# Kernel optimization log

Measured on AMD Instinct MI355X. Metric: run time of the kernel, lower is better.

## Reference

```python
import jax, jax.numpy as jnp
import numpy as np

DIM_Q = 512
DIM_K = 512
DIM_V = 512
NUM_HEADS = 8
LN_EPS = 1e-5


def setup_inputs() -> dict:
    key = jax.random.key(0)
    ks = jax.random.split(key, 12)
    s_q = 1.0 / np.sqrt(DIM_Q)
    s_k = 1.0 / np.sqrt(DIM_K)
    s_v = 1.0 / np.sqrt(DIM_V)
    return {
        "Q": jax.random.normal(ks[0], (8, 1024, DIM_Q), dtype=jnp.float32),
        "K": jax.random.normal(ks[1], (8, 1024, DIM_K), dtype=jnp.float32),
        "Wq": jax.random.uniform(ks[2], (DIM_Q, DIM_V), jnp.float32, -s_q, s_q),
        "bq": jax.random.uniform(ks[3], (DIM_V,), jnp.float32, -s_q, s_q),
        "Wk": jax.random.uniform(ks[4], (DIM_K, DIM_V), jnp.float32, -s_k, s_k),
        "bk": jax.random.uniform(ks[5], (DIM_V,), jnp.float32, -s_k, s_k),
        "Wv": jax.random.uniform(ks[6], (DIM_K, DIM_V), jnp.float32, -s_k, s_k),
        "bv": jax.random.uniform(ks[7], (DIM_V,), jnp.float32, -s_k, s_k),
        "Wo": jax.random.uniform(ks[8], (DIM_V, DIM_V), jnp.float32, -s_v, s_v),
        "bo": jax.random.uniform(ks[9], (DIM_V,), jnp.float32, -s_v, s_v),
        "g0": jnp.ones((DIM_V,), jnp.float32),
        "b0": jnp.zeros((DIM_V,), jnp.float32),
        "g1": jnp.ones((DIM_V,), jnp.float32),
        "b1": jnp.zeros((DIM_V,), jnp.float32),
    }


def _layer_norm(x, gamma, beta):
    mu = jnp.mean(x, axis=-1, keepdims=True)
    var = jnp.var(x, axis=-1, keepdims=True)
    return (x - mu) * jax.lax.rsqrt(var + LN_EPS) * gamma + beta


def reference(Q, K, Wq, bq, Wk, bk, Wv, bv, Wo, bo, g0, b0, g1, b1):
    B, Nq, _ = Q.shape
    Nk = K.shape[1]
    H = NUM_HEADS
    d = DIM_V // H  # head dim

    Qp = Q @ Wq + bq                      # [B, Nq, dim_V]
    Kp = K @ Wk + bk                      # [B, Nk, dim_V]
    Vp = K @ Wv + bv                      # [B, Nk, dim_V]

    Qh = Qp.reshape(B, Nq, H, d)
    Kh = Kp.reshape(B, Nk, H, d)
    Vh = Vp.reshape(B, Nk, H, d)

    scores = jnp.einsum("bqhd,bkhd->bhqk", Qh, Kh) / jnp.sqrt(jnp.float32(d))
    A = jax.nn.softmax(scores, axis=-1)   # [B, H, Nq, Nk]
    Oh = jnp.einsum("bhqk,bkhd->bqhd", A, Vh) + Qh  # residual with projected Q
    O = Oh.reshape(B, Nq, DIM_V)

    O = _layer_norm(O, g0, b0)
    O = O + jax.nn.relu(O @ Wo + bo)
    O = _layer_norm(O, g1, b1)
    return O
```

## Files before the change

### kernel.cpp

```cpp
#include <hip/hip_runtime.h>
#include <math.h>

#define DV 512
#define HD 64
#define NHEADS 8
#define SEQ 1024
#define NBATCH 8
#define MROWS (NBATCH * SEQ)

typedef __bf16 bf16;
typedef __bf16 bf16x8 __attribute__((ext_vector_type(8)));
typedef __bf16 bf16x4 __attribute__((ext_vector_type(4)));
typedef float f32x4 __attribute__((ext_vector_type(4)));

__device__ inline void gload_lds16(const void* g, void* l) {
  __builtin_amdgcn_global_load_lds(
      (const __attribute__((address_space(1))) unsigned int*)g,
      (__attribute__((address_space(3))) unsigned int*)l, 16, 0, 0);
}

__device__ __forceinline__ bf16x8 cvt8(float4 a, float4 b) {
  bf16x8 o;
  o[0] = (bf16)a.x; o[1] = (bf16)a.y; o[2] = (bf16)a.z; o[3] = (bf16)a.w;
  o[4] = (bf16)b.x; o[5] = (bf16)b.y; o[6] = (bf16)b.z; o[7] = (bf16)b.w;
  return o;
}

__global__ __launch_bounds__(256) void prep_w(
    const float* __restrict__ W0, const float* __restrict__ W1,
    const float* __restrict__ W2, const float* __restrict__ W3,
    bf16* __restrict__ T0, bf16* __restrict__ T1,
    bf16* __restrict__ T2, bf16* __restrict__ T3)
{
  const int z = blockIdx.z;
  const float* W = z == 0 ? W0 : z == 1 ? W1 : z == 2 ? W2 : W3;
  bf16* WT = z == 0 ? T0 : z == 1 ? T1 : z == 2 ? T2 : T3;
  __shared__ float T[64][65];
  const int t = threadIdx.x;
  const int k0 = (blockIdx.x >> 3) * 64, n0 = (blockIdx.x & 7) * 64;
#pragma unroll
  for (int p = 0; p < 4; ++p) {
    int r = p * 16 + (t >> 4), c = (t & 15) * 4;
    float4 v = *(const float4*)&W[(size_t)(k0 + r) * DV + n0 + c];
    T[r][c] = v.x; T[r][c + 1] = v.y; T[r][c + 2] = v.z; T[r][c + 3] = v.w;
  }
  __syncthreads();
#pragma unroll
  for (int p = 0; p < 2; ++p) {
    int n = p * 32 + (t >> 3), kc = (t & 7) * 8;
    bf16x8 o;
#pragma unroll
    for (int j = 0; j < 8; ++j) o[j] = (bf16)T[kc + j][n];
    *(bf16x8*)&WT[(size_t)(n0 + n) * DV + k0 + kc] = o;
  }
}

template<bool SA>
__device__ __forceinline__ void proj_core(
    const float* __restrict__ Sg, const bf16* __restrict__ Wg,
    int s0, int w0, float* Sf, bf16* Wb, f32x4 (*acc)[4])
{
  const int tid = threadIdx.x;
  const int lane = tid & 63, w = tid >> 6;
  const int wm = w >> 1, wn = w & 1;
  const int cl = lane & 15, qd = lane >> 4;
  const int sw = SA ? wm : wn;
  const int ww = SA ? wn : wm;

  size_t offS[4]; int uS[4];
#pragma unroll
  for (int t = 0; t < 4; ++t) {
    int S = t * 256 + tid;
    int row = S >> 3, g = (S & 7) ^ (row & 7);
    offS[t] = (size_t)(s0 + row) * DV + g * 4;
    uS[t] = (t * 256 + w * 64) * 4;
  }
  size_t offW[2]; int uW[2];
#pragma unroll
  for (int t = 0; t < 2; ++t) {
    int S = t * 256 + tid;
    int row = S >> 2, g = (S & 3) ^ ((row >> 1) & 3);
    offW[t] = (size_t)(w0 + row) * DV + g * 8;
    uW[t] = (t * 256 + w * 64) * 8;
  }

#pragma unroll
  for (int t = 0; t < 4; ++t) gload_lds16(Sg + offS[t], Sf + uS[t]);
#pragma unroll
  for (int t = 0; t < 2; ++t) gload_lds16(Wg + offW[t], Wb + uW[t]);

  for (int it = 0; it < 16; ++it) {
    __syncthreads();
    const int cur = it & 1;
    if (it + 1 < 16) {
      const size_t kn = (size_t)(it + 1) * 32;
#pragma unroll
      for (int t = 0; t < 4; ++t)
        gload_lds16(Sg + kn + offS[t], Sf + (cur ^ 1) * 4096 + uS[t]);
#pragma unroll
      for (int t = 0; t < 2; ++t)
        gload_lds16(Wg + kn + offW[t], Wb + (cur ^ 1) * 4096 + uW[t]);
    }
    const float* S_ = Sf + cur * 4096;
    const bf16* W_ = Wb + cur * 4096;

    bf16x8 sf[4], wf[4];
#pragma unroll
    for (int j = 0; j < 4; ++j) {
      int row = sw * 64 + j * 16 + cl;
      int lo = row * 8 + ((2 * qd) ^ (row & 7));
      int hi = row * 8 + ((2 * qd + 1) ^ (row & 7));
      float4 a = *(const float4*)(S_ + lo * 4);
      float4 b = *(const float4*)(S_ + hi * 4);
      sf[j] = cvt8(a, b);
    }
#pragma unroll
    for (int j = 0; j < 4; ++j) {
      int row = ww * 64 + j * 16 + cl;
      int slot = row * 4 + (qd ^ ((row >> 1) & 3));
      wf[j] = *(const bf16x8*)(W_ + (size_t)slot * 8);
    }
#pragma unroll
    for (int mi = 0; mi < 4; ++mi)
#pragma unroll
      for (int ni = 0; ni < 4; ++ni) {
        if (SA)
          acc[mi][ni] = __builtin_amdgcn_mfma_f32_16x16x32_bf16(
              sf[mi], wf[ni], acc[mi][ni], 0, 0, 0);
        else
          acc[mi][ni] = __builtin_amdgcn_mfma_f32_16x16x32_bf16(
              wf[mi], sf[ni], acc[mi][ni], 0, 0, 0);
      }
  }
}

__global__ __launch_bounds__(256) void gemm_proj(
    const float* __restrict__ Qf, const float* __restrict__ Kf,
    const bf16* __restrict__ WqT, const bf16* __restrict__ WkT,
    const bf16* __restrict__ WvT,
    const float* __restrict__ bq, const float* __restrict__ bk,
    const float* __restrict__ bv,
    bf16* __restrict__ Qp, bf16* __restrict__ Kp, bf16* __restrict__ VpT)
{
  __shared__ float Sf[2 * 4096];
  __shared__ bf16 Wb[2 * 4096];
  const int z = blockIdx.z;
  int m0, n0, N;
  f32x4 acc[4][4] = {};
  if (z < 2) {
    m0 = (blockIdx.x & 63) * 128; n0 = (blockIdx.x >> 6) * 128; N = DV;
    proj_core<true>(z ? Kf : Qf, z ? WkT : WqT, m0, n0, Sf, Wb, acc);
  } else {
    n0 = (blockIdx.x & 63) * 128; m0 = (blockIdx.x >> 6) * 128; N = MROWS;
    proj_core<false>(Kf, WvT, n0, m0, Sf, Wb, acc);
  }

  const float* bias = z == 0 ? bq : z == 1 ? bk : bv;
  bf16* C = z == 0 ? Qp : z == 1 ? Kp : VpT;
  const int lane = threadIdx.x & 63, w = threadIdx.x >> 6;
  const int wm = w >> 1, wn = w & 1;
  const int cl = lane & 15, qd = lane >> 4;
  float bcol[4] = {0.f, 0.f, 0.f, 0.f};
  if (z < 2)
#pragma unroll
    for (int ni = 0; ni < 4; ++ni) bcol[ni] = bias[n0 + wn * 64 + ni * 16 + cl];
#pragma unroll
  for (int mi = 0; mi < 4; ++mi)
#pragma unroll
    for (int r = 0; r < 4; ++r) {
      int gm = m0 + wm * 64 + mi * 16 + qd * 4 + r;
      float brow = (z == 2) ? bias[gm] : 0.f;
#pragma unroll
      for (int ni = 0; ni < 4; ++ni) {
        int gn = n0 + wn * 64 + ni * 16 + cl;
        float v = acc[mi][ni][r] + (z == 2 ? brow : bcol[ni]);
        C[(size_t)gm * N + gn] = (bf16)v;
      }
    }
}

__global__ __launch_bounds__(256) void attn_mfma(
    const bf16* __restrict__ Qp, const bf16* __restrict__ Kp,
    const bf16* __restrict__ VpT, bf16* __restrict__ Orb)
{
  __shared__ bf16 Ks[2][64 * 64];
  __shared__ bf16 Vs[2][64 * 64];
  __shared__ bf16 Ps[4][32 * 72];

  const int tid = threadIdx.x, lane = tid & 63, w = tid >> 6;
  const int cl = lane & 15, qd = lane >> 4;
  const int bh = blockIdx.x, b = bh >> 3, h = bh & 7;
  const int q0w = blockIdx.y * 128 + w * 32;

  const float SCL = 0.18033688011112042f;
  bf16x8 qa[2][2];
#pragma unroll
  for (int qt = 0; qt < 2; ++qt)
#pragma unroll
    for (int ch = 0; ch < 2; ++ch) {
      bf16x8 v = *(const bf16x8*)(Qp + ((size_t)b * SEQ + q0w + qt * 16 + cl) * DV
                                  + h * HD + ch * 32 + qd * 8);
#pragma unroll
      for (int j = 0; j < 8; ++j) v[j] = (bf16)((float)v[j] * SCL);
      qa[qt][ch] = v;
    }

  f32x4 o[4][2] = {};
  float lrun[2] = {0.f, 0.f};

  const bf16* Kbase = Kp + (size_t)b * SEQ * DV + h * HD;
  const bf16* Vbase = VpT + (size_t)h * HD * MROWS + (size_t)b * SEQ;
  bf16* Pw = &Ps[w][0];

  const int Sa = tid, Sb = 256 + tid;
  const int kRowA = Sa >> 3, kDgA = (Sa & 7) ^ (kRowA & 7);
  const int kRowB = Sb >> 3, kDgB = (Sb & 7) ^ (kRowB & 7);
  const size_t kOffA = (size_t)kRowA * DV + kDgA * 8;
  const size_t kOffB = (size_t)kRowB * DV + kDgB * 8;
  const size_t vOffA = (size_t)kRowA * MROWS + kDgA * 8;
  const size_t vOffB = (size_t)kRowB * MROWS + kDgB * 8;

  gload_lds16(Kbase + kOffA, &Ks[0][(size_t)(w * 64) * 8]);
  gload_lds16(Kbase + kOffB, &Ks[0][(size_t)(256 + w * 64) * 8]);
  gload_lds16(Vbase + vOffA, &Vs[0][(size_t)(w * 64) * 8]);
  gload_lds16(Vbase + vOffB, &Vs[0][(size_t)(256 + w * 64) * 8]);

  for (int it = 0; it < SEQ / 64; ++it) {
    __syncthreads();
    const int cur = it & 1;
    if (it + 1 < SEQ / 64) {
      const size_t kt = (size_t)(it + 1) * 64;
      gload_lds16(Kbase + kt * DV + kOffA, &Ks[cur ^ 1][(size_t)(w * 64) * 8]);
      gload_lds16(Kbase + kt * DV + kOffB, &Ks[cur ^ 1][(size_t)(256 + w * 64) * 8]);
      gload_lds16(Vbase + kt + vOffA, &Vs[cur ^ 1][(size_t)(w * 64) * 8]);
      gload_lds16(Vbase + kt + vOffB, &Vs[cur ^ 1][(size_t)(256 + w * 64) * 8]);
    }
    const bf16* K_ = &Ks[cur][0];
    const bf16* V_ = &Vs[cur][0];

    f32x4 sc[4][2] = {};
#pragma unroll
    for (int ch = 0; ch < 2; ++ch) {
      bf16x8 kf[4];
#pragma unroll
      for (int kt4 = 0; kt4 < 4; ++kt4) {
        int key = kt4 * 16 + cl;
        int slot = key * 8 + ((ch * 4 + qd) ^ (key & 7));
        kf[kt4] = *(const bf16x8*)(K_ + (size_t)slot * 8);
      }
#pragma unroll
      for (int kt4 = 0; kt4 < 4; ++kt4)
#pragma unroll
        for (int qt = 0; qt < 2; ++qt)
          sc[kt4][qt] = __builtin_amdgcn_mfma_f32_16x16x32_bf16(
              kf[kt4], qa[qt][ch], sc[kt4][qt], 0, 0, 0);
    }

#pragma unroll
    for (int qt = 0; qt < 2; ++qt) {
      float sum = 0.f;
#pragma unroll
      for (int kt4 = 0; kt4 < 4; ++kt4) {
        float p0 = __builtin_amdgcn_exp2f(sc[kt4][qt][0]);
        float p1 = __builtin_amdgcn_exp2f(sc[kt4][qt][1]);
        float p2 = __builtin_amdgcn_exp2f(sc[kt4][qt][2]);
        float p3 = __builtin_amdgcn_exp2f(sc[kt4][qt][3]);
        sum += (p0 + p1) + (p2 + p3);
        bf16x4 pk;
        pk[0] = (bf16)p0; pk[1] = (bf16)p1; pk[2] = (bf16)p2; pk[3] = (bf16)p3;
        *(bf16x4*)(Pw + (size_t)(qt * 16 + cl) * 72 + kt4 * 16 + qd * 4) = pk;
      }
      sum += __shfl_xor(sum, 16);
      sum += __shfl_xor(sum, 32);
      lrun[qt] += sum;
    }

#pragma unroll
    for (int kc = 0; kc < 2; ++kc) {
      bf16x8 pb[2];
#pragma unroll
      for (int qt = 0; qt < 2; ++qt)
        pb[qt] = *(const bf16x8*)(Pw + (size_t)(qt * 16 + cl) * 72 + kc * 32 + qd * 8);
#pragma unroll
      for (int dt = 0; dt < 4; ++dt) {
        int d = dt * 16 + cl;
        int slot = d * 8 + ((kc * 4 + qd) ^ (d & 7));
        bf16x8 vf = *(const bf16x8*)(V_ + (size_t)slot * 8);
#pragma unroll
        for (int qt = 0; qt < 2; ++qt)
          o[dt][qt] = __builtin_amdgcn_mfma_f32_16x16x32_bf16(
              vf, pb[qt], o[dt][qt], 0, 0, 0);
      }
    }
  }

#pragma unroll
  for (int qt = 0; qt < 2; ++qt) {
    float inv = 1.f / lrun[qt];
    size_t rowoff = ((size_t)b * SEQ + q0w + qt * 16 + cl) * DV + h * HD;
#pragma unroll
    for (int dt = 0; dt < 4; ++dt) {
      bf16x4 rv = *(const bf16x4*)(Qp + rowoff + dt * 16 + qd * 4);
      bf16x4 st;
      st[0] = (bf16)(o[dt][qt][0] * inv + (float)rv[0]);
      st[1] = (bf16)(o[dt][qt][1] * inv + (float)rv[1]);
      st[2] = (bf16)(o[dt][qt][2] * inv + (float)rv[2]);
      st[3] = (bf16)(o[dt][qt][3] * inv + (float)rv[3]);
      *(bf16x4*)(Orb + rowoff + dt * 16 + qd * 4) = st;
    }
  }
}

__global__ __launch_bounds__(256) void gemm_fused(
    const bf16* __restrict__ Orb, const bf16* __restrict__ WoT,
    const float* __restrict__ bo,
    const float* __restrict__ g0, const float* __restrict__ b0,
    const float* __restrict__ g1, const float* __restrict__ b1,
    float* __restrict__ out)
{
  __shared__ bf16 Bsm[32 * 512];
  __shared__ bf16 As[2][2048 * 8];
  const int tid = threadIdx.x, lane = tid & 63, w = tid >> 6;
  const int cl = lane & 15, qd = lane >> 4;
  const int m0 = blockIdx.x * 32;

  size_t offA[8];
  int uOff[8];
#pragma unroll
  for (int t = 0; t < 8; ++t) {
    int S = t * 256 + tid;
    int frow = S >> 2, kq = (S & 3) ^ ((frow >> 1) & 3);
    offA[t] = (size_t)frow * DV + kq * 8;
    uOff[t] = (t * 256 + w * 64) * 8;
  }

#pragma unroll
  for (int t = 0; t < 8; ++t)
    gload_lds16(WoT + offA[t], As[0] + uOff[t]);

  {
    const int q = tid >> 3, c0 = (tid & 7) * 64;
    const bf16* src = Orb + (size_t)(m0 + q) * DV + c0;
    float x[64];
    float s = 0.f, s2 = 0.f;
#pragma unroll
    for (int j = 0; j < 8; ++j) {
      bf16x8 xv = *(const bf16x8*)(src + j * 8);
#pragma unroll
      for (int e = 0; e < 8; ++e) {
        float f = (float)xv[e];
        x[j * 8 + e] = f; s += f; s2 += f * f;
      }
    }
    s  += __shfl_xor(s, 1);  s  += __shfl_xor(s, 2);  s  += __shfl_xor(s, 4);
    s2 += __shfl_xor(s2, 1); s2 += __shfl_xor(s2, 2); s2 += __shfl_xor(s2, 4);
    float mu = s * (1.f / DV);
    float inv = rsqrtf(s2 * (1.f / DV) - mu * mu + 1e-5f);
#pragma unroll
    for (int j = 0; j < 8; ++j) {
      float4 ga = *(const float4*)(g0 + c0 + j * 8);
      float4 gb = *(const float4*)(g0 + c0 + j * 8 + 4);
      float4 ba = *(const float4*)(b0 + c0 + j * 8);
      float4 bb = *(const float4*)(b0 + c0 + j * 8 + 4);
      bf16x8 o;
      o[0] = (bf16)((x[j*8+0] - mu) * inv * ga.x + ba.x);
      o[1] = (bf16)((x[j*8+1] - mu) * inv * ga.y + ba.y);
      o[2] = (bf16)((x[j*8+2] - mu) * inv * ga.z + ba.z);
      o[3] = (bf16)((x[j*8+3] - mu) * inv * ga.w + ba.w);
      o[4] = (bf16)((x[j*8+4] - mu) * inv * gb.x + bb.x);
      o[5] = (bf16)((x[j*8+5] - mu) * inv * gb.y + bb.y);
      o[6] = (bf16)((x[j*8+6] - mu) * inv * gb.z + bb.z);
      o[7] = (bf16)((x[j*8+7] - mu) * inv * gb.w + bb.w);
      int g = (tid & 7) * 8 + j;
      int slot = q * 64 + (g ^ (q & 7));
      *(bf16x8*)(Bsm + (size_t)slot * 8) = o;
    }
  }

  f32x4 acc[8][2] = {};
  for (int it = 0; it < 16; ++it) {
    __syncthreads();
    const int cur = it & 1;
    if (it + 1 < 16) {
#pragma unroll
      for (int t = 0; t < 8; ++t)
        gload_lds16(WoT + (size_t)(it + 1) * 32 + offA[t], As[cur ^ 1] + uOff[t]);
    }
    bf16x8 bfr[2];
#pragma unroll
    for (int nt = 0; nt < 2; ++nt) {
      int q = nt * 16 + cl;
      int slot = q * 64 + ((it * 4 + qd) ^ (q & 7));
      bfr[nt] = *(const bf16x8*)(Bsm + (size_t)slot * 8);
    }
#pragma unroll
    for (int mt = 0; mt < 8; ++mt) {
      int frow = (w * 8 + mt) * 16 + cl;
      int slot = frow * 4 + (qd ^ ((frow >> 1) & 3));
      bf16x8 af = *(const bf16x8*)(As[cur] + (size_t)slot * 8);
#pragma unroll
      for (int nt = 0; nt < 2; ++nt)
        acc[mt][nt] = __builtin_amdgcn_mfma_f32_16x16x32_bf16(
            af, bfr[nt], acc[mt][nt], 0, 0, 0);
    }
  }

  __syncthreads();
  float* red = (float*)As;
  float y[8][2][4];
  float sy[2], sy2[2];
#pragma unroll
  for (int nt = 0; nt < 2; ++nt) {
    sy[nt] = 0.f; sy2[nt] = 0.f;
    const int q = nt * 16 + cl;
#pragma unroll
    for (int mt = 0; mt < 8; ++mt) {
      const int f0 = (w * 8 + mt) * 16 + qd * 4;
      float4 bov = *(const float4*)(bo + f0);
      int g = f0 >> 3;
      int slot = q * 64 + (g ^ (q & 7));
      bf16x4 rv = *(const bf16x4*)(Bsm + (size_t)slot * 8 + (qd & 1) * 4);
      const float* bp = (const float*)&bov;
#pragma unroll
      for (int r = 0; r < 4; ++r) {
        float v = fmaxf(acc[mt][nt][r] + bp[r], 0.f) + (float)rv[r];
        y[mt][nt][r] = v;
        sy[nt] += v; sy2[nt] += v * v;
      }
    }
    sy[nt]  += __shfl_xor(sy[nt], 16);  sy[nt]  += __shfl_xor(sy[nt], 32);
    sy2[nt] += __shfl_xor(sy2[nt], 16); sy2[nt] += __shfl_xor(sy2[nt], 32);
  }
  if (qd == 0) {
#pragma unroll
    for (int nt = 0; nt < 2; ++nt) {
      int q = nt * 16 + cl;
      red[(q * 4 + w) * 2 + 0] = sy[nt];
      red[(q * 4 + w) * 2 + 1] = sy2[nt];
    }
  }
  __syncthreads();
#pragma unroll
  for (int nt = 0; nt < 2; ++nt) {
    const int q = nt * 16 + cl;
    float s = 0.f, s2 = 0.f;
#pragma unroll
    for (int ww = 0; ww < 4; ++ww) {
      s  += red[(q * 4 + ww) * 2 + 0];
      s2 += red[(q * 4 + ww) * 2 + 1];
    }
    float mu1 = s * (1.f / DV);
    float inv1 = rsqrtf(s2 * (1.f / DV) - mu1 * mu1 + 1e-5f);
    size_t rowoff = (size_t)(m0 + q) * DV;
#pragma unroll
    for (int mt = 0; mt < 8; ++mt) {
      const int f0 = (w * 8 + mt) * 16 + qd * 4;
      float4 gv = *(const float4*)(g1 + f0);
      float4 bv = *(const float4*)(b1 + f0);
      float4 ov;
      ov.x = (y[mt][nt][0] - mu1) * inv1 * gv.x + bv.x;
      ov.y = (y[mt][nt][1] - mu1) * inv1 * gv.y + bv.y;
      ov.z = (y[mt][nt][2] - mu1) * inv1 * gv.z + bv.z;
      ov.w = (y[mt][nt][3] - mu1) * inv1 * gv.w + bv.w;
      *(float4*)(out + rowoff + f0) = ov;
    }
  }
}

extern "C" void kernel_launch(void* const* d_in, const int* in_sizes, int n_in,
                              void* d_out, int out_size, void* d_ws, size_t ws_size,
                              hipStream_t stream)
{
  const float* Q  = (const float*)d_in[0];
  const float* Kf = (const float*)d_in[1];
  const float* Wq = (const float*)d_in[2];
  const float* bq = (const float*)d_in[3];
  const float* Wk = (const float*)d_in[4];
  const float* bk = (const float*)d_in[5];
  const float* Wv = (const float*)d_in[6];
  const float* bv = (const float*)d_in[7];
  const float* Wo = (const float*)d_in[8];
  const float* bo = (const float*)d_in[9];
  const float* g0 = (const float*)d_in[10];
  const float* b0 = (const float*)d_in[11];
  const float* g1 = (const float*)d_in[12];
  const float* b1 = (const float*)d_in[13];
  float* out = (float*)d_out;

  const size_t MB = 1ull << 20;
  char* W = (char*)d_ws;
  bf16* Orb = (bf16*)(W + 0);
  bf16* Qp  = (bf16*)(W + 8 * MB);
  bf16* Kp  = (bf16*)(W + 16 * MB);
  bf16* VpT = (bf16*)(W + 24 * MB);
  bf16* WqT = (bf16*)(W + 32 * MB);
  bf16* WkT = (bf16*)(W + 32 * MB + 512 * 1024);
  bf16* WvT = (bf16*)(W + 33 * MB);
  bf16* WoT = (bf16*)(W + 33 * MB + 512 * 1024);

  dim3 blk(256);
  prep_w<<<dim3(64, 1, 4), blk, 0, stream>>>(Wq, Wk, Wv, Wo, WqT, WkT, WvT, WoT);
  gemm_proj<<<dim3(256, 1, 3), blk, 0, stream>>>(
      Q, Kf, WqT, WkT, WvT, bq, bk, bv, Qp, Kp, VpT);
  attn_mfma<<<dim3(NBATCH * NHEADS, SEQ / 128), blk, 0, stream>>>(Qp, Kp, VpT, Orb);
  gemm_fused<<<dim3(MROWS / 32), blk, 0, stream>>>(
      Orb, WoT, bo, g0, b0, g1, b1, out);
}
```

Before: 188.8 us.

## Fuse K and V projections into one block sharing the K input tile

The K and V projections are merged into the same thread block, so each K tile is loaded from global memory and converted to bf16 once and then feeds both the Wk and Wv products. The grid drops from three z-slices to two, and z=1 blocks do twice the MFMA work with a second accumulator set and a second LDS weight buffer. This removes redundant reads and conversions of K, but it doubles accumulator registers (which may hurt occupancy) and leaves an imbalance between z=0 and z=1 blocks.

```diff
diff --git a/kernel.cpp b/kernel.cpp
--- a/kernel.cpp
+++ b/kernel.cpp
@@ -55,85 +55,6 @@
   }
 }
 
-template<bool SA>
-__device__ __forceinline__ void proj_core(
-    const float* __restrict__ Sg, const bf16* __restrict__ Wg,
-    int s0, int w0, float* Sf, bf16* Wb, f32x4 (*acc)[4])
-{
-  const int tid = threadIdx.x;
-  const int lane = tid & 63, w = tid >> 6;
-  const int wm = w >> 1, wn = w & 1;
-  const int cl = lane & 15, qd = lane >> 4;
-  const int sw = SA ? wm : wn;
-  const int ww = SA ? wn : wm;
-
-  size_t offS[4]; int uS[4];
-#pragma unroll
-  for (int t = 0; t < 4; ++t) {
-    int S = t * 256 + tid;
-    int row = S >> 3, g = (S & 7) ^ (row & 7);
-    offS[t] = (size_t)(s0 + row) * DV + g * 4;
-    uS[t] = (t * 256 + w * 64) * 4;
-  }
-  size_t offW[2]; int uW[2];
-#pragma unroll
-  for (int t = 0; t < 2; ++t) {
-    int S = t * 256 + tid;
-    int row = S >> 2, g = (S & 3) ^ ((row >> 1) & 3);
-    offW[t] = (size_t)(w0 + row) * DV + g * 8;
-    uW[t] = (t * 256 + w * 64) * 8;
-  }
-
-#pragma unroll
-  for (int t = 0; t < 4; ++t) gload_lds16(Sg + offS[t], Sf + uS[t]);
-#pragma unroll
-  for (int t = 0; t < 2; ++t) gload_lds16(Wg + offW[t], Wb + uW[t]);
-
-  for (int it = 0; it < 16; ++it) {
-    __syncthreads();
-    const int cur = it & 1;
-    if (it + 1 < 16) {
-      const size_t kn = (size_t)(it + 1) * 32;
-#pragma unroll
-      for (int t = 0; t < 4; ++t)
-        gload_lds16(Sg + kn + offS[t], Sf + (cur ^ 1) * 4096 + uS[t]);
-#pragma unroll
-      for (int t = 0; t < 2; ++t)
-        gload_lds16(Wg + kn + offW[t], Wb + (cur ^ 1) * 4096 + uW[t]);
-    }
-    const float* S_ = Sf + cur * 4096;
-    const bf16* W_ = Wb + cur * 4096;
-
-    bf16x8 sf[4], wf[4];
-#pragma unroll
-    for (int j = 0; j < 4; ++j) {
-      int row = sw * 64 + j * 16 + cl;
-      int lo = row * 8 + ((2 * qd) ^ (row & 7));
-      int hi = row * 8 + ((2 * qd + 1) ^ (row & 7));
-      float4 a = *(const float4*)(S_ + lo * 4);
-      float4 b = *(const float4*)(S_ + hi * 4);
-      sf[j] = cvt8(a, b);
-    }
-#pragma unroll
-    for (int j = 0; j < 4; ++j) {
-      int row = ww * 64 + j * 16 + cl;
-      int slot = row * 4 + (qd ^ ((row >> 1) & 3));
-      wf[j] = *(const bf16x8*)(W_ + (size_t)slot * 8);
-    }
-#pragma unroll
-    for (int mi = 0; mi < 4; ++mi)
-#pragma unroll
-      for (int ni = 0; ni < 4; ++ni) {
-        if (SA)
-          acc[mi][ni] = __builtin_amdgcn_mfma_f32_16x16x32_bf16(
-              sf[mi], wf[ni], acc[mi][ni], 0, 0, 0);
-        else
-          acc[mi][ni] = __builtin_amdgcn_mfma_f32_16x16x32_bf16(
-              wf[mi], sf[ni], acc[mi][ni], 0, 0, 0);
-      }
-  }
-}
-
 __global__ __launch_bounds__(256) void gemm_proj(
     const float* __restrict__ Qf, const float* __restrict__ Kf,
     const bf16* __restrict__ WqT, const bf16* __restrict__ WkT,
@@ -143,40 +64,138 @@
     bf16* __restrict__ Qp, bf16* __restrict__ Kp, bf16* __restrict__ VpT)
 {
   __shared__ float Sf[2 * 4096];
-  __shared__ bf16 Wb[2 * 4096];
+  __shared__ bf16 W1[2 * 4096];
+  __shared__ bf16 W2[2 * 4096];
   const int z = blockIdx.z;
-  int m0, n0, N;
-  f32x4 acc[4][4] = {};
-  if (z < 2) {
-    m0 = (blockIdx.x & 63) * 128; n0 = (blockIdx.x >> 6) * 128; N = DV;
-    proj_core<true>(z ? Kf : Qf, z ? WkT : WqT, m0, n0, Sf, Wb, acc);
-  } else {
-    n0 = (blockIdx.x & 63) * 128; m0 = (blockIdx.x >> 6) * 128; N = MROWS;
-    proj_core<false>(Kf, WvT, n0, m0, Sf, Wb, acc);
-  }
-
-  const float* bias = z == 0 ? bq : z == 1 ? bk : bv;
-  bf16* C = z == 0 ? Qp : z == 1 ? Kp : VpT;
-  const int lane = threadIdx.x & 63, w = threadIdx.x >> 6;
+  const int tid = threadIdx.x;
+  const int lane = tid & 63, w = tid >> 6;
   const int wm = w >> 1, wn = w & 1;
   const int cl = lane & 15, qd = lane >> 4;
-  float bcol[4] = {0.f, 0.f, 0.f, 0.f};
-  if (z < 2)
-#pragma unroll
-    for (int ni = 0; ni < 4; ++ni) bcol[ni] = bias[n0 + wn * 64 + ni * 16 + cl];
-#pragma unroll
-  for (int mi = 0; mi < 4; ++mi)
-#pragma unroll
-    for (int r = 0; r < 4; ++r) {
-      int gm = m0 + wm * 64 + mi * 16 + qd * 4 + r;
-      float brow = (z == 2) ? bias[gm] : 0.f;
-#pragma unroll
-      for (int ni = 0; ni < 4; ++ni) {
-        int gn = n0 + wn * 64 + ni * 16 + cl;
-        float v = acc[mi][ni][r] + (z == 2 ? brow : bcol[ni]);
-        C[(size_t)gm * N + gn] = (bf16)v;
-      }
-    }
+  const int s0 = (blockIdx.x & 63) * 128;
+  const int w0 = (blockIdx.x >> 6) * 128;
+
+  const float* Sg = z ? Kf : Qf;
+  const bf16* Wg1 = z ? WkT : WqT;
+
+  size_t offS[4]; int uS[4];
+#pragma unroll
+  for (int t = 0; t < 4; ++t) {
+    int S = t * 256 + tid;
+    int row = S >> 3, g = (S & 7) ^ (row & 7);
+    offS[t] = (size_t)(s0 + row) * DV + g * 4;
+    uS[t] = (t * 256 + w * 64) * 4;
+  }
+  size_t offW[2]; int uW[2];
+#pragma unroll
+  for (int t = 0; t < 2; ++t) {
+    int S = t * 256 + tid;
+    int row = S >> 2, g = (S & 3) ^ ((row >> 1) & 3);
+    offW[t] = (size_t)(w0 + row) * DV + g * 8;
+    uW[t] = (t * 256 + w * 64) * 8;
+  }
+
+#pragma unroll
+  for (int t = 0; t < 4; ++t) gload_lds16(Sg + offS[t], Sf + uS[t]);
+#pragma unroll
+  for (int t = 0; t < 2; ++t) gload_lds16(Wg1 + offW[t], W1 + uW[t]);
+  if (z)
+#pragma unroll
+    for (int t = 0; t < 2; ++t) gload_lds16(WvT + offW[t], W2 + uW[t]);
+
+  f32x4 acc1[4][4] = {};
+  f32x4 acc2[4][4] = {};
+
+  for (int it = 0; it < 16; ++it) {
+    __syncthreads();
+    const int cur = it & 1;
+    if (it + 1 < 16) {
+      const size_t kn = (size_t)(it + 1) * 32;
+#pragma unroll
+      for (int t = 0; t < 4; ++t)
+        gload_lds16(Sg + kn + offS[t], Sf + (cur ^ 1) * 4096 + uS[t]);
+#pragma unroll
+      for (int t = 0; t < 2; ++t)
+        gload_lds16(Wg1 + kn + offW[t], W1 + (cur ^ 1) * 4096 + uW[t]);
+      if (z)
+#pragma unroll
+        for (int t = 0; t < 2; ++t)
+          gload_lds16(WvT + kn + offW[t], W2 + (cur ^ 1) * 4096 + uW[t]);
+    }
+    const float* S_ = Sf + cur * 4096;
+    const bf16* W1_ = W1 + cur * 4096;
+    const bf16* W2_ = W2 + cur * 4096;
+
+    bf16x8 sf[4], w1f[4];
+#pragma unroll
+    for (int j = 0; j < 4; ++j) {
+      int row = wm * 64 + j * 16 + cl;
+      int lo = row * 8 + ((2 * qd) ^ (row & 7));
+      int hi = row * 8 + ((2 * qd + 1) ^ (row & 7));
+      float4 a = *(const float4*)(S_ + lo * 4);
+      float4 b = *(const float4*)(S_ + hi * 4);
+      sf[j] = cvt8(a, b);
+    }
+#pragma unroll
+    for (int j = 0; j < 4; ++j) {
+      int row = wn * 64 + j * 16 + cl;
+      int slot = row * 4 + (qd ^ ((row >> 1) & 3));
+      w1f[j] = *(const bf16x8*)(W1_ + (size_t)slot * 8);
+    }
+#pragma unroll
+    for (int mi = 0; mi < 4; ++mi)
+#pragma unroll
+      for (int ni = 0; ni < 4; ++ni)
+        acc1[mi][ni] = __builtin_amdgcn_mfma_f32_16x16x32_bf16(
+            sf[mi], w1f[ni], acc1[mi][ni], 0, 0, 0);
+    if (z) {
+      bf16x8 w2f[4];
+#pragma unroll
+      for (int j = 0; j < 4; ++j) {
+        int row = wn * 64 + j * 16 + cl;
+        int slot = row * 4 + (qd ^ ((row >> 1) & 3));
+        w2f[j] = *(const bf16x8*)(W2_ + (size_t)slot * 8);
+      }
+#pragma unroll
+      for (int mi = 0; mi < 4; ++mi)
+#pragma unroll
+        for (int ni = 0; ni < 4; ++ni)
+          acc2[mi][ni] = __builtin_amdgcn_mfma_f32_16x16x32_bf16(
+              w2f[mi], sf[ni], acc2[mi][ni], 0, 0, 0);
+    }
+  }
+
+  {
+    const float* bias = z ? bk : bq;
+    bf16* C = z ? Kp : Qp;
+    float bcol[4];
+#pragma unroll
+    for (int ni = 0; ni < 4; ++ni) bcol[ni] = bias[w0 + wn * 64 + ni * 16 + cl];
+#pragma unroll
+    for (int mi = 0; mi < 4; ++mi)
+#pragma unroll
+      for (int r = 0; r < 4; ++r) {
+        int gm = s0 + wm * 64 + mi * 16 + qd * 4 + r;
+#pragma unroll
+        for (int ni = 0; ni < 4; ++ni) {
+          int gn = w0 + wn * 64 + ni * 16 + cl;
+          C[(size_t)gm * DV + gn] = (bf16)(acc1[mi][ni][r] + bcol[ni]);
+        }
+      }
+  }
+  if (z) {
+#pragma unroll
+    for (int mi = 0; mi < 4; ++mi)
+#pragma unroll
+      for (int r = 0; r < 4; ++r) {
+        int gm = w0 + wn * 64 + mi * 16 + qd * 4 + r;
+        float brow = bv[gm];
+#pragma unroll
+        for (int ni = 0; ni < 4; ++ni) {
+          int gn = s0 + wm * 64 + ni * 16 + cl;
+          VpT[(size_t)gm * MROWS + gn] = (bf16)(acc2[mi][ni][r] + brow);
+        }
+      }
+  }
 }
 
 __global__ __launch_bounds__(256) void attn_mfma(
@@ -500,7 +519,7 @@
 
   dim3 blk(256);
   prep_w<<<dim3(64, 1, 4), blk, 0, stream>>>(Wq, Wk, Wv, Wo, WqT, WkT, WvT, WoT);
-  gemm_proj<<<dim3(256, 1, 3), blk, 0, stream>>>(
+  gemm_proj<<<dim3(256, 1, 2), blk, 0, stream>>>(
       Q, Kf, WqT, WkT, WvT, bq, bk, bv, Qp, Kp, VpT);
   attn_mfma<<<dim3(NBATCH * NHEADS, SEQ / 128), blk, 0, stream>>>(Qp, Kp, VpT, Orb);
   gemm_fused<<<dim3(MROWS / 32), blk, 0, stream>>>(
```

Measured after the change: 192.8 us. +2.1%, slower.
